# Kernel optimization log

Measured on AMD Instinct MI355X. Metric: run time of the kernel, lower is better.

Reference implementation:

```python
import jax, jax.numpy as jnp
import numpy as np

EMBED_DIM = 512
NUM_HEADS = 8
D_HEAD = EMBED_DIM // NUM_HEADS  # 64
BLOCK = 64
SEQ = 8192
BATCH = 2
N_GLOBAL = 2
N_WINDOW = 3
N_RANDOM = 3
NB = SEQ // BLOCK  # 128 blocks
M = N_GLOBAL + N_WINDOW + N_RANDOM  # gathered key blocks per query block


def setup_inputs() -> dict:
    key = jax.random.key(0)
    ks = jax.random.split(key, 12)
    s = 0.05  # ~xavier scale for [512,64]
    return {
        "query": jax.random.normal(ks[0], (SEQ, BATCH, EMBED_DIM), jnp.float32),
        "key_inp": jax.random.normal(ks[1], (SEQ, BATCH, EMBED_DIM), jnp.float32),
        "value": jax.random.normal(ks[2], (SEQ, BATCH, EMBED_DIM), jnp.float32),
        "q_w": jax.random.normal(ks[3], (NUM_HEADS, EMBED_DIM, D_HEAD), jnp.float32) * s,
        "k_w": jax.random.normal(ks[4], (NUM_HEADS, EMBED_DIM, D_HEAD), jnp.float32) * s,
        "v_w": jax.random.normal(ks[5], (NUM_HEADS, EMBED_DIM, D_HEAD), jnp.float32) * s,
        "q_b": jnp.zeros((NUM_HEADS, D_HEAD), jnp.float32),
        "k_b": jnp.zeros((NUM_HEADS, D_HEAD), jnp.float32),
        "v_b": jnp.zeros((NUM_HEADS, D_HEAD), jnp.float32),
        "out_w": jax.random.normal(ks[6], (EMBED_DIM, EMBED_DIM), jnp.float32) * 0.04,
        "out_b": jnp.zeros((EMBED_DIM,), jnp.float32),
        "rand_idx": jax.random.randint(ks[7], (NB, N_RANDOM), 0, NB, dtype=jnp.int32),
    }


def _gather_block_idx(rand_idx):
    # per query block: global blocks + sliding window (mod NB) + random blocks -> [NB, M]
    glob = jnp.broadcast_to(jnp.arange(N_GLOBAL, dtype=jnp.int32), (NB, N_GLOBAL))
    half = N_WINDOW // 2
    win = (jnp.arange(NB, dtype=jnp.int32)[:, None]
           + jnp.arange(N_WINDOW, dtype=jnp.int32)[None, :] - half) % NB
    return jnp.concatenate([glob, win, rand_idx], axis=1)


def _sparse_attn(Q, K, V, rand_idx):
    # Q,K,V: [B,H,S,dh] -> out [B,H,S,dh]
    B, H, S, dh = Q.shape
    Qb = Q.reshape(B, H, NB, BLOCK, dh)
    Kb = K.reshape(B, H, NB, BLOCK, dh)
    Vb = V.reshape(B, H, NB, BLOCK, dh)
    idx = _gather_block_idx(rand_idx)              # [NB, M]
    Kg = Kb[:, :, idx]                              # [B,H,NB,M,BLOCK,dh]
    Vg = Vb[:, :, idx].reshape(B, H, NB, M * BLOCK, dh)
    scores = jnp.einsum('bhnqd,bhnmkd->bhnqmk', Qb, Kg) / jnp.sqrt(jnp.float32(dh))
    scores = scores.reshape(B, H, NB, BLOCK, M * BLOCK)
    attn = jax.nn.softmax(scores, axis=-1)
    out = jnp.einsum('bhnqk,bhnkd->bhnqd', attn, Vg)
    return out.reshape(B, H, S, dh)


def reference(query, key_inp, value, q_w, k_w, v_w, q_b, k_b, v_b, out_w, out_b, rand_idx):
    # batch_first=False: [S,B,E] -> [B,S,E]
    q = jnp.transpose(query, (1, 0, 2))
    k = jnp.transpose(key_inp, (1, 0, 2))
    v = jnp.transpose(value, (1, 0, 2))
    # per-head projections: [B,S,E] x [H,E,dh] -> [B,H,S,dh]
    Q = jnp.einsum('bse,hed->bhsd', q, q_w) + q_b[None, :, None, :]
    K = jnp.einsum('bse,hed->bhsd', k, k_w) + k_b[None, :, None, :]
    V = jnp.einsum('bse,hed->bhsd', v, v_w) + v_b[None, :, None, :]
    ao = _sparse_attn(Q, K, V, rand_idx)            # [B,H,S,dh]
    flat = jnp.transpose(ao, (0, 2, 1, 3)).reshape(BATCH * SEQ, EMBED_DIM)
    out = flat @ out_w.T + out_b                    # nn.Linear
    out = out.reshape(BATCH, SEQ, EMBED_DIM)
    return jnp.transpose(out, (1, 0, 2))            # back to [S,B,E]
```

## Files before the change

### kernel.cpp

```cpp
#include <hip/hip_runtime.h>
#include <stdint.h>

#define NBLK 128
#define KDIM 512

typedef __attribute__((ext_vector_type(8))) short short8;
typedef __attribute__((ext_vector_type(4))) float f32x4;
typedef unsigned short u16;

__device__ __forceinline__ u16 f2bf(float f) {
  unsigned u = __float_as_uint(f);
  u = u + 0x7fffu + ((u >> 16) & 1u);
  return (u16)(u >> 16);
}

__device__ __forceinline__ void g2l16(const void* g, void* l) {
  __builtin_amdgcn_global_load_lds(
      (__attribute__((address_space(1))) void*)(g),
      (__attribute__((address_space(3))) void*)(l), 16, 0, 0);
}

__global__ void conv_inputs(const float* __restrict__ q, const float* __restrict__ k,
                            const float* __restrict__ v, u16* __restrict__ qb,
                            u16* __restrict__ kb, u16* __restrict__ vb) {
  const float* src[3] = {q, k, v};
  u16* dst[3] = {qb, kb, vb};
  int t = blockIdx.x * 256 + threadIdx.x;
  int o = t * 4;
  int b = o >> 22;
  int s = (o >> 9) & 8191;
  int e = o & 511;
  float4 val = *(const float4*)(src[blockIdx.y] + ((s * 2 + b) * 512 + e));
  ushort4 r;
  r.x = f2bf(val.x); r.y = f2bf(val.y); r.z = f2bf(val.z); r.w = f2bf(val.w);
  *(ushort4*)(dst[blockIdx.y] + o) = r;
}

__global__ void prep_weights(const float* __restrict__ qw, const float* __restrict__ kw,
                             const float* __restrict__ vw, const float* __restrict__ ow,
                             u16* __restrict__ wqt, u16* __restrict__ wkt,
                             u16* __restrict__ wvt, u16* __restrict__ owb) {
  int t = blockIdx.x * 256 + threadIdx.x;
  int y = blockIdx.y;
  if (y < 3) {
    const float* w = (y == 0) ? qw : (y == 1) ? kw : vw;
    u16* dstp = (y == 0) ? wqt : (y == 1) ? wkt : wvt;
    int c = t >> 7;
    int e4 = (t & 127) * 4;
    int h = c >> 6, d = c & 63;
    const float* base = w + h * (512 * 64) + d;
    ushort4 r;
    r.x = f2bf(base[(e4 + 0) * 64]);
    r.y = f2bf(base[(e4 + 1) * 64]);
    r.z = f2bf(base[(e4 + 2) * 64]);
    r.w = f2bf(base[(e4 + 3) * 64]);
    *(ushort4*)(dstp + c * 512 + e4) = r;
  } else {
    float4 val = *(const float4*)(ow + t * 4);
    ushort4 r;
    r.x = f2bf(val.x); r.y = f2bf(val.y); r.z = f2bf(val.z); r.w = f2bf(val.w);
    *(ushort4*)(owb + t * 4) = r;
  }
}

template <int MODE>
__global__ __launch_bounds__(256, 2)
void gemm_bt(const u16* __restrict__ A, const u16* __restrict__ BT,
             const float* __restrict__ bias, void* __restrict__ dstv) {
  __shared__ u16 As[128 * 32];
  __shared__ u16 Bs[128 * 32];
  const int t = threadIdx.x;
  const int lane = t & 63, w = t >> 6;
  const int l15 = lane & 15, quad = lane >> 4;
  const int wm = w >> 1, wn = w & 1;
  const int tileM = blockIdx.y * 128, tileN = blockIdx.x * 128;

  f32x4 acc[4][4];
#pragma unroll
  for (int i = 0; i < 4; ++i)
#pragma unroll
    for (int j = 0; j < 4; ++j) acc[i][j] = (f32x4){0.f, 0.f, 0.f, 0.f};

  const int c1 = t, c2 = t + 256;
  const u16* gA1 = A + (tileM + (c1 >> 2)) * KDIM + (c1 & 3) * 8;
  const u16* gA2 = A + (tileM + (c2 >> 2)) * KDIM + (c2 & 3) * 8;
  const u16* gB1 = BT + (tileN + (c1 >> 2)) * KDIM + (c1 & 3) * 8;
  const u16* gB2 = BT + (tileN + (c2 >> 2)) * KDIM + (c2 & 3) * 8;
  u16* lA1 = As + c1 * 8; u16* lA2 = As + c2 * 8;
  u16* lB1 = Bs + c1 * 8; u16* lB2 = Bs + c2 * 8;

  for (int k0 = 0; k0 < KDIM; k0 += 32) {
    __syncthreads();
    g2l16(gA1 + k0, lA1);
    g2l16(gA2 + k0, lA2);
    g2l16(gB1 + k0, lB1);
    g2l16(gB2 + k0, lB2);
    __syncthreads();
    short8 af[4], bfr[4];
#pragma unroll
    for (int mt = 0; mt < 4; ++mt)
      af[mt] = *(const short8*)(As + (wm * 64 + mt * 16 + l15) * 32 + quad * 8);
#pragma unroll
    for (int nt = 0; nt < 4; ++nt)
      bfr[nt] = *(const short8*)(Bs + (wn * 64 + nt * 16 + l15) * 32 + quad * 8);
#pragma unroll
    for (int mt = 0; mt < 4; ++mt)
#pragma unroll
      for (int nt = 0; nt < 4; ++nt)
        acc[mt][nt] = __builtin_amdgcn_mfma_f32_16x16x32_bf16(af[mt], bfr[nt], acc[mt][nt], 0, 0, 0);
  }

#pragma unroll
  for (int mt = 0; mt < 4; ++mt) {
#pragma unroll
    for (int nt = 0; nt < 4; ++nt) {
      const int n = tileN + wn * 64 + nt * 16 + l15;
#pragma unroll
      for (int r = 0; r < 4; ++r) {
        const int m = tileM + wm * 64 + mt * 16 + quad * 4 + r;
        float val = acc[mt][nt][r];
        if (MODE == 0) {
          val += bias[n];
          int b = m >> 13, s = m & 8191, h = n >> 6, d = n & 63;
          ((u16*)dstv)[((b * 8 + h) * 8192 + s) * 64 + d] = f2bf(val);
        } else if (MODE == 1) {
          val += bias[m];
          int h = m >> 6, d = m & 63, b = n >> 13, s = n & 8191;
          ((u16*)dstv)[(b * 512 + h * 64 + d) * 8192 + s] = f2bf(val);
        } else {
          val += bias[n];
          int s = m & 8191, b = m >> 13;
          ((float*)dstv)[(s * 2 + b) * 512 + n] = val;
        }
      }
    }
  }
}

__global__ __launch_bounds__(256, 4)
void attn(const u16* __restrict__ Qb, const u16* __restrict__ Kb,
          const u16* __restrict__ Vt, const int* __restrict__ ridx,
          u16* __restrict__ AO) {
  __shared__ u16 Ks[64 * 64];
  __shared__ u16 Vs[64 * 64];
  __shared__ u16 Ps[64 * 64];
  const int blk = blockIdx.x;
  const int bh = blk & 15, nb = blk >> 4;
  const int b = bh >> 3, h = bh & 7;
  const int t = threadIdx.x, lane = t & 63, w = t >> 6;
  const int l15 = lane & 15, quad = lane >> 4;

  int bidx[8];
  bidx[0] = 0; bidx[1] = 1;
  bidx[2] = (nb + NBLK - 1) & (NBLK - 1);
  bidx[3] = nb;
  bidx[4] = (nb + 1) & (NBLK - 1);
  bidx[5] = ridx[nb * 3 + 0];
  bidx[6] = ridx[nb * 3 + 1];
  bidx[7] = ridx[nb * 3 + 2];

  const u16* qrow = Qb + (bh * 8192 + nb * 64 + w * 16 + l15) * 64;
  short8 aq0 = *(const short8*)(qrow + quad * 8);
  short8 aq1 = *(const short8*)(qrow + 32 + quad * 8);

  const int s0 = t, s1 = t + 256;
  const int r0 = s0 >> 3, c0 = (s0 & 7) ^ (r0 & 7);
  const int r1 = s1 >> 3, c1 = (s1 & 7) ^ (r1 & 7);
  const u16* Kbase = Kb + bh * 8192 * 64;
  const u16* Vbase = Vt + (bh * 64) * 8192;

  f32x4 oacc[4];
#pragma unroll
  for (int i = 0; i < 4; ++i) oacc[i] = (f32x4){0.f, 0.f, 0.f, 0.f};
  float lsum[4] = {0.f, 0.f, 0.f, 0.f};

  for (int m = 0; m < 8; ++m) {
    const int kb0 = bidx[m] * 64;
    __syncthreads();
    g2l16(Kbase + (kb0 + r0) * 64 + c0 * 8, Ks + s0 * 8);
    g2l16(Kbase + (kb0 + r1) * 64 + c1 * 8, Ks + s1 * 8);
    g2l16(Vbase + r0 * 8192 + kb0 + c0 * 8, Vs + s0 * 8);
    g2l16(Vbase + r1 * 8192 + kb0 + c1 * 8, Vs + s1 * 8);
    __syncthreads();

    f32x4 s[4];
#pragma unroll
    for (int i = 0; i < 4; ++i) s[i] = (f32x4){0.f, 0.f, 0.f, 0.f};
#pragma unroll
    for (int nt = 0; nt < 4; ++nt) {
      const int key = nt * 16 + l15;
      const u16* kr = Ks + key * 64;
      short8 bk0 = *(const short8*)(kr + ((quad ^ (key & 7)) << 3));
      short8 bk1 = *(const short8*)(kr + (((4 + quad) ^ (key & 7)) << 3));
      s[nt] = __builtin_amdgcn_mfma_f32_16x16x32_bf16(aq0, bk0, s[nt], 0, 0, 0);
      s[nt] = __builtin_amdgcn_mfma_f32_16x16x32_bf16(aq1, bk1, s[nt], 0, 0, 0);
    }

#pragma unroll
    for (int nt = 0; nt < 4; ++nt) {
      const int key = nt * 16 + l15;
      const int cp = key >> 3;
#pragma unroll
      for (int rr = 0; rr < 4; ++rr) {
        float p = __expf(s[nt][rr] * 0.125f);
        lsum[rr] += p;
        const int q = w * 16 + quad * 4 + rr;
        Ps[q * 64 + (((cp ^ (q & 7)) << 3) | (key & 7))] = f2bf(p);
      }
    }

    const int q2 = w * 16 + l15;
    const u16* pr = Ps + q2 * 64;
    short8 ap0 = *(const short8*)(pr + ((quad ^ (q2 & 7)) << 3));
    short8 ap1 = *(const short8*)(pr + (((4 + quad) ^ (q2 & 7)) << 3));
#pragma unroll
    for (int nt = 0; nt < 4; ++nt) {
      const int d = nt * 16 + l15;
      const u16* vr = Vs + d * 64;
      short8 bv0 = *(const short8*)(vr + ((quad ^ (d & 7)) << 3));
      short8 bv1 = *(const short8*)(vr + (((4 + quad) ^ (d & 7)) << 3));
      oacc[nt] = __builtin_amdgcn_mfma_f32_16x16x32_bf16(ap0, bv0, oacc[nt], 0, 0, 0);
      oacc[nt] = __builtin_amdgcn_mfma_f32_16x16x32_bf16(ap1, bv1, oacc[nt], 0, 0, 0);
    }
  }

#pragma unroll
  for (int msk = 1; msk < 16; msk <<= 1)
#pragma unroll
    for (int rr = 0; rr < 4; ++rr) lsum[rr] += __shfl_xor(lsum[rr], msk, 64);
  float inv[4];
#pragma unroll
  for (int rr = 0; rr < 4; ++rr) inv[rr] = __builtin_amdgcn_rcpf(lsum[rr]);

#pragma unroll
  for (int nt = 0; nt < 4; ++nt) {
    const int cc = h * 64 + nt * 16 + l15;
#pragma unroll
    for (int rr = 0; rr < 4; ++rr) {
      const int s = nb * 64 + w * 16 + quad * 4 + rr;
      AO[(b * 8192 + s) * 512 + cc] = f2bf(oacc[nt][rr] * inv[rr]);
    }
  }
}

extern "C" void kernel_launch(void* const* d_in, const int* in_sizes, int n_in,
                              void* d_out, int out_size, void* d_ws, size_t ws_size,
                              hipStream_t stream) {
  const float* q   = (const float*)d_in[0];
  const float* k   = (const float*)d_in[1];
  const float* v   = (const float*)d_in[2];
  const float* qw  = (const float*)d_in[3];
  const float* kw  = (const float*)d_in[4];
  const float* vw  = (const float*)d_in[5];
  const float* qbi = (const float*)d_in[6];
  const float* kbi = (const float*)d_in[7];
  const float* vbi = (const float*)d_in[8];
  const float* ow  = (const float*)d_in[9];
  const float* ob  = (const float*)d_in[10];
  const int*   ri  = (const int*)d_in[11];

  char* ws = (char*)d_ws;
  const size_t MB1 = 1024 * 1024;
  u16* qbuf = (u16*)(ws + 0);
  u16* kbuf = (u16*)(ws + 16 * MB1);
  u16* vbuf = (u16*)(ws + 32 * MB1);
  u16* AO   = (u16*)(ws + 0);
  u16* Qb   = (u16*)(ws + 48 * MB1);
  u16* Kb   = (u16*)(ws + 64 * MB1);
  u16* Vt   = (u16*)(ws + 80 * MB1);
  u16* WqT  = (u16*)(ws + 96 * MB1);
  u16* WkT  = (u16*)(ws + 96 * MB1 + 512 * 1024);
  u16* WvT  = (u16*)(ws + 97 * MB1);
  u16* OW   = (u16*)(ws + 97 * MB1 + 512 * 1024);

  conv_inputs<<<dim3(8192, 3), 256, 0, stream>>>(q, k, v, qbuf, kbuf, vbuf);
  prep_weights<<<dim3(256, 4), 256, 0, stream>>>(qw, kw, vw, ow, WqT, WkT, WvT, OW);
  gemm_bt<0><<<dim3(4, 128), 256, 0, stream>>>(qbuf, WqT, qbi, Qb);
  gemm_bt<0><<<dim3(4, 128), 256, 0, stream>>>(kbuf, WkT, kbi, Kb);
  gemm_bt<1><<<dim3(128, 4), 256, 0, stream>>>(WvT, vbuf, vbi, Vt);
  attn<<<2048, 256, 0, stream>>>(Qb, Kb, Vt, ri, AO);
  gemm_bt<2><<<dim3(4, 128), 256, 0, stream>>>(AO, OW, ob, d_out);
}
```

Baseline: 265.4 us.

## Merge QKV GEMMs, swizzle LDS tiles, stage epilogue through LDS for vector stores

The three projection GEMMs become a single launch with a z-dimension and a remapped tile order. LDS tiles now use an XOR swizzle to reduce bank conflicts. Epilogues write results through swizzled shared memory so that global stores are 16-byte vectors instead of scattered scalar stores, which matters most for the transposed V output and the fp32 output. Occupancy hints also change for the GEMM and attention kernels, and the larger shared-memory buffer may reduce occupancy.

```diff
diff --git a/kernel.cpp b/kernel.cpp
--- a/kernel.cpp
+++ b/kernel.cpp
@@ -64,16 +64,15 @@
 }
 
 template <int MODE>
-__global__ __launch_bounds__(256, 2)
-void gemm_bt(const u16* __restrict__ A, const u16* __restrict__ BT,
-             const float* __restrict__ bias, void* __restrict__ dstv) {
-  __shared__ u16 As[128 * 32];
-  __shared__ u16 Bs[128 * 32];
+__device__ __forceinline__ void gemm_core(const u16* __restrict__ A, const u16* __restrict__ BT,
+                                          const float* __restrict__ bias, void* __restrict__ dstv,
+                                          int tileM, int tileN, u16* sh) {
   const int t = threadIdx.x;
   const int lane = t & 63, w = t >> 6;
   const int l15 = lane & 15, quad = lane >> 4;
   const int wm = w >> 1, wn = w & 1;
-  const int tileM = blockIdx.y * 128, tileN = blockIdx.x * 128;
+  u16* As = sh;
+  u16* Bs = sh + 4096;
 
   f32x4 acc[4][4];
 #pragma unroll
@@ -81,63 +80,128 @@
 #pragma unroll
     for (int j = 0; j < 4; ++j) acc[i][j] = (f32x4){0.f, 0.f, 0.f, 0.f};
 
-  const int c1 = t, c2 = t + 256;
-  const u16* gA1 = A + (tileM + (c1 >> 2)) * KDIM + (c1 & 3) * 8;
-  const u16* gA2 = A + (tileM + (c2 >> 2)) * KDIM + (c2 & 3) * 8;
-  const u16* gB1 = BT + (tileN + (c1 >> 2)) * KDIM + (c1 & 3) * 8;
-  const u16* gB2 = BT + (tileN + (c2 >> 2)) * KDIM + (c2 & 3) * 8;
-  u16* lA1 = As + c1 * 8; u16* lA2 = As + c2 * 8;
-  u16* lB1 = Bs + c1 * 8; u16* lB2 = Bs + c2 * 8;
+  const int s0 = t, s1 = t + 256;
+  const int r0 = s0 >> 2, g0 = (s0 & 3) ^ (r0 & 3);
+  const int r1 = s1 >> 2, g1 = (s1 & 3) ^ (r1 & 3);
+  const u16* gA0 = A + (tileM + r0) * KDIM + g0 * 8;
+  const u16* gA1 = A + (tileM + r1) * KDIM + g1 * 8;
+  const u16* gB0 = BT + (tileN + r0) * KDIM + g0 * 8;
+  const u16* gB1 = BT + (tileN + r1) * KDIM + g1 * 8;
 
   for (int k0 = 0; k0 < KDIM; k0 += 32) {
     __syncthreads();
-    g2l16(gA1 + k0, lA1);
-    g2l16(gA2 + k0, lA2);
-    g2l16(gB1 + k0, lB1);
-    g2l16(gB2 + k0, lB2);
-    __syncthreads();
-    short8 af[4], bfr[4];
+    g2l16(gA0 + k0, As + s0 * 8);
+    g2l16(gA1 + k0, As + s1 * 8);
+    g2l16(gB0 + k0, Bs + s0 * 8);
+    g2l16(gB1 + k0, Bs + s1 * 8);
+    __syncthreads();
+    short8 af[4], bf[4];
+#pragma unroll
+    for (int mt = 0; mt < 4; ++mt) {
+      const int ra = wm * 64 + mt * 16 + l15;
+      af[mt] = *(const short8*)(As + ra * 32 + ((quad ^ (ra & 3)) << 3));
+    }
+#pragma unroll
+    for (int nt = 0; nt < 4; ++nt) {
+      const int rb = wn * 64 + nt * 16 + l15;
+      bf[nt] = *(const short8*)(Bs + rb * 32 + ((quad ^ (rb & 3)) << 3));
+    }
 #pragma unroll
     for (int mt = 0; mt < 4; ++mt)
-      af[mt] = *(const short8*)(As + (wm * 64 + mt * 16 + l15) * 32 + quad * 8);
-#pragma unroll
-    for (int nt = 0; nt < 4; ++nt)
-      bfr[nt] = *(const short8*)(Bs + (wn * 64 + nt * 16 + l15) * 32 + quad * 8);
+#pragma unroll
+      for (int nt = 0; nt < 4; ++nt)
+        acc[mt][nt] = __builtin_amdgcn_mfma_f32_16x16x32_bf16(af[mt], bf[nt], acc[mt][nt], 0, 0, 0);
+  }
+  __syncthreads();
+
+  if (MODE == 0 || MODE == 1) {
 #pragma unroll
     for (int mt = 0; mt < 4; ++mt)
 #pragma unroll
       for (int nt = 0; nt < 4; ++nt)
-        acc[mt][nt] = __builtin_amdgcn_mfma_f32_16x16x32_bf16(af[mt], bfr[nt], acc[mt][nt], 0, 0, 0);
-  }
-
-#pragma unroll
-  for (int mt = 0; mt < 4; ++mt) {
-#pragma unroll
-    for (int nt = 0; nt < 4; ++nt) {
-      const int n = tileN + wn * 64 + nt * 16 + l15;
-#pragma unroll
-      for (int r = 0; r < 4; ++r) {
-        const int m = tileM + wm * 64 + mt * 16 + quad * 4 + r;
-        float val = acc[mt][nt][r];
-        if (MODE == 0) {
-          val += bias[n];
-          int b = m >> 13, s = m & 8191, h = n >> 6, d = n & 63;
-          ((u16*)dstv)[((b * 8 + h) * 8192 + s) * 64 + d] = f2bf(val);
-        } else if (MODE == 1) {
-          val += bias[m];
-          int h = m >> 6, d = m & 63, b = n >> 13, s = n & 8191;
-          ((u16*)dstv)[(b * 512 + h * 64 + d) * 8192 + s] = f2bf(val);
-        } else {
-          val += bias[n];
-          int s = m & 8191, b = m >> 13;
-          ((float*)dstv)[(s * 2 + b) * 512 + n] = val;
+#pragma unroll
+        for (int r = 0; r < 4; ++r) {
+          const int lrow = wm * 64 + mt * 16 + quad * 4 + r;
+          const int col = wn * 64 + nt * 16 + l15;
+          float v = acc[mt][nt][r] + (MODE == 0 ? bias[tileN + col] : bias[tileM + lrow]);
+          const int ch = col >> 3;
+          sh[lrow * 128 + ((ch ^ (lrow & 7)) << 3) + (col & 7)] = f2bf(v);
         }
+    __syncthreads();
+#pragma unroll
+    for (int p = 0; p < 8; ++p) {
+      const int idx = p * 256 + t;
+      const int row = idx >> 4, c = idx & 15;
+      short8 vch = *(const short8*)(sh + row * 128 + ((c ^ (row & 7)) << 3));
+      if (MODE == 0) {
+        const int m = tileM + row, b = m >> 13, s = m & 8191;
+        const int n0 = tileN + c * 8, h = n0 >> 6, d = n0 & 63;
+        *(short8*)((u16*)dstv + (((b * 8 + h) * 8192 + s) * 64 + d)) = vch;
+      } else {
+        const int hd = tileM + row;
+        const int n0 = tileN + c * 8, b = n0 >> 13, s = n0 & 8191;
+        *(short8*)((u16*)dstv + ((b * 512 + hd) * 8192 + s)) = vch;
       }
     }
-  }
-}
-
-__global__ __launch_bounds__(256, 4)
+  } else {
+    float* Cf = (float*)sh;
+#pragma unroll
+    for (int half = 0; half < 2; ++half) {
+      if (wm == half) {
+#pragma unroll
+        for (int mt = 0; mt < 4; ++mt)
+#pragma unroll
+          for (int nt = 0; nt < 4; ++nt)
+#pragma unroll
+            for (int r = 0; r < 4; ++r) {
+              const int lrow = mt * 16 + quad * 4 + r;
+              const int col = wn * 64 + nt * 16 + l15;
+              float v = acc[mt][nt][r] + bias[tileN + col];
+              const int ch = col >> 2;
+              Cf[lrow * 128 + ((ch ^ ((lrow & 7) << 2)) << 2) + (col & 3)] = v;
+            }
+      }
+      __syncthreads();
+#pragma unroll
+      for (int p = 0; p < 8; ++p) {
+        const int idx = p * 256 + t;
+        const int row = idx >> 5, c = idx & 31;
+        float4 v4 = *(const float4*)(Cf + row * 128 + ((c ^ ((row & 7) << 2)) << 2));
+        const int m = tileM + half * 64 + row;
+        const int s = m & 8191, b = m >> 13;
+        *(float4*)((float*)dstv + ((s * 2 + b) * 512 + tileN + c * 4)) = v4;
+      }
+      __syncthreads();
+    }
+  }
+}
+
+__global__ __launch_bounds__(256, 3)
+void gemm_qkv(const u16* __restrict__ qb, const u16* __restrict__ kb, const u16* __restrict__ vb,
+              const u16* __restrict__ WqT, const u16* __restrict__ WkT, const u16* __restrict__ WvT,
+              const float* __restrict__ qbi, const float* __restrict__ kbi, const float* __restrict__ vbi,
+              u16* __restrict__ Qb, u16* __restrict__ Kb, u16* __restrict__ Vt) {
+  __shared__ u16 sh[16384];
+  const int id = blockIdx.x + blockIdx.y * 4;
+  const int xs = (id >> 3) & 3;
+  const int ys = (id & 7) * 16 + (id >> 5);
+  const int z = blockIdx.z;
+  if (z == 0)      gemm_core<0>(qb, WqT, qbi, Qb, ys * 128, xs * 128, sh);
+  else if (z == 1) gemm_core<0>(kb, WkT, kbi, Kb, ys * 128, xs * 128, sh);
+  else             gemm_core<1>(WvT, vb, vbi, Vt, xs * 128, ys * 128, sh);
+}
+
+__global__ __launch_bounds__(256, 3)
+void gemm_out_k(const u16* __restrict__ AO, const u16* __restrict__ OW,
+                const float* __restrict__ ob, float* __restrict__ out) {
+  __shared__ u16 sh[16384];
+  const int id = blockIdx.x + blockIdx.y * 4;
+  const int xs = (id >> 3) & 3;
+  const int ys = (id & 7) * 16 + (id >> 5);
+  gemm_core<2>(AO, OW, ob, out, ys * 128, xs * 128, sh);
+}
+
+__global__ __launch_bounds__(256, 5)
 void attn(const u16* __restrict__ Qb, const u16* __restrict__ Kb,
           const u16* __restrict__ Vt, const int* __restrict__ ridx,
           u16* __restrict__ AO) {
@@ -275,9 +339,8 @@
 
   conv_inputs<<<dim3(8192, 3), 256, 0, stream>>>(q, k, v, qbuf, kbuf, vbuf);
   prep_weights<<<dim3(256, 4), 256, 0, stream>>>(qw, kw, vw, ow, WqT, WkT, WvT, OW);
-  gemm_bt<0><<<dim3(4, 128), 256, 0, stream>>>(qbuf, WqT, qbi, Qb);
-  gemm_bt<0><<<dim3(4, 128), 256, 0, stream>>>(kbuf, WkT, kbi, Kb);
-  gemm_bt<1><<<dim3(128, 4), 256, 0, stream>>>(WvT, vbuf, vbi, Vt);
+  gemm_qkv<<<dim3(4, 128, 3), 256, 0, stream>>>(qbuf, kbuf, vbuf, WqT, WkT, WvT,
+                                                qbi, kbi, vbi, Qb, Kb, Vt);
   attn<<<2048, 256, 0, stream>>>(Qb, Kb, Vt, ri, AO);
-  gemm_bt<2><<<dim3(4, 128), 256, 0, stream>>>(AO, OW, ob, d_out);
-}
+  gemm_out_k<<<dim3(4, 128), 256, 0, stream>>>(AO, OW, ob, (float*)d_out);
+}
```

Result: faster. 252.4 us (-4.9%).
